# Performance work log

Measured on AMD Instinct MI355X. Metric: run time of the kernel, lower is better.

## Reference

```python
import jax, jax.numpy as jnp
import numpy as np

B, S, D, H, HD = 4, 2048, 1024, 16, 64


def setup_inputs() -> dict:
    key = jax.random.key(0)
    k1, k2, k3 = jax.random.split(key, 3)
    x = jax.random.normal(k1, (B, S, D), dtype=jnp.float32)
    w_attn = jax.random.normal(k2, (D, 3, H, HD), dtype=jnp.float32) * 0.02
    b_attn = jnp.zeros((3, H, HD), dtype=jnp.float32)
    w_proj = jax.random.normal(k3, (H, HD, D), dtype=jnp.float32) * 0.02
    b_proj = jnp.zeros((D,), dtype=jnp.float32)
    return {"x": x, "w_attn": w_attn, "b_attn": b_attn, "w_proj": w_proj, "b_proj": b_proj}


def reference(x, w_attn, b_attn, w_proj, b_proj):
    # c_attn: [B,S,D] x [D,3,H,HD] -> [B,3,H,S,HD]
    qkv = jnp.einsum('bsd,dqhe->bqhse', x, w_attn) + b_attn[None, :, :, None, :]
    q, k, v = qkv[:, 0], qkv[:, 1], qkv[:, 2]  # each [B,H,S,HD]
    scale = 1.0 / jnp.sqrt(jnp.asarray(HD, dtype=q.dtype))
    scores = jnp.einsum('bhse,bhte->bhst', q * scale, k)  # [B,H,S,S]
    causal = jnp.tril(jnp.ones((S, S), dtype=bool))
    scores = jnp.where(causal, scores, jnp.asarray(-1e9, dtype=scores.dtype))
    attn = jax.nn.softmax(scores, axis=-1)
    out = jnp.einsum('bhst,bhte->bhse', attn, v)  # [B,H,S,HD]
    # c_proj: contract (heads, head_size) -> embed
    return jnp.einsum('bhse,hed->bsd', out, w_proj) + b_proj
```

## Files before the change

### kernel.cpp

```cpp
#include <hip/hip_runtime.h>

#define NB 4
#define NS 2048
#define ND 1024
#define NH 16
#define NE 64
#define NM (NB*NS)

typedef __attribute__((ext_vector_type(8))) __bf16 bf16x8;
typedef __attribute__((ext_vector_type(4))) float f32x4;

__device__ __forceinline__ float bf2f(unsigned short h) {
  union { unsigned u; float f; } c; c.u = ((unsigned)h) << 16; return c.f;
}
__device__ __forceinline__ unsigned short f2bf(float f) {
  union { float f; unsigned u; } c; c.f = f;
  return (unsigned short)((c.u + 0x7fffu + ((c.u >> 16) & 1u)) >> 16);
}
__device__ __forceinline__ void load16_to_lds(const void* g, void* l) {
  __builtin_amdgcn_global_load_lds(
      (__attribute__((address_space(1))) void*)(void*)(unsigned long long)(const char*)g,
      (__attribute__((address_space(3))) void*)l, 16, 0, 0);
}

__global__ void detect_dtype(const unsigned* __restrict__ x, int* __restrict__ flag) {
  __shared__ int cnt;
  if (threadIdx.x == 0) cnt = 0;
  __syncthreads();
  unsigned w = x[((unsigned)threadIdx.x * 16381u) & ((1u << 21) - 1u)];
  unsigned lo = w & 0xFFFFu;
  int e = (int)((lo >> 7) & 0xFF);
  int plausible = (lo == 0u) || (e >= 100 && e <= 142);
  atomicAdd(&cnt, plausible);
  __syncthreads();
  if (threadIdx.x == 0) *flag = (cnt >= 192) ? 1 : 0;
}

__global__ void conv_to_bf16(const void* __restrict__ src, unsigned short* __restrict__ dst,
                             int n, const int* __restrict__ flag) {
  int stride = gridDim.x * blockDim.x;
  int i0 = blockIdx.x * blockDim.x + threadIdx.x;
  if (*flag) {
    const unsigned short* s = (const unsigned short*)src;
    for (int i = i0; i < n; i += stride) dst[i] = s[i];
  } else {
    const float* s = (const float*)src;
    for (int i = i0; i < n; i += stride) dst[i] = f2bf(s[i]);
  }
}

__global__ __launch_bounds__(256) void transpose_conv(const void* __restrict__ in,
                                                      unsigned short* __restrict__ out,
                                                      int K, int N, const int* __restrict__ flag) {
  __shared__ unsigned short tile[32][33];
  int n0 = blockIdx.x * 32, k0 = blockIdx.y * 32;
  int tx = threadIdx.x, ty = threadIdx.y;
  if (*flag) {
    const unsigned short* p = (const unsigned short*)in;
#pragma unroll
    for (int i = 0; i < 4; ++i)
      tile[ty + 8*i][tx] = p[(size_t)(k0 + ty + 8*i) * N + n0 + tx];
  } else {
    const float* p = (const float*)in;
#pragma unroll
    for (int i = 0; i < 4; ++i)
      tile[ty + 8*i][tx] = f2bf(p[(size_t)(k0 + ty + 8*i) * N + n0 + tx]);
  }
  __syncthreads();
#pragma unroll
  for (int i = 0; i < 4; ++i)
    out[(size_t)(n0 + ty + 8*i) * K + k0 + tx] = tile[tx][ty + 8*i];
}

#define SLOT_ELEMS ((256 + 128) * 64)

__device__ __forceinline__ void gemm_core_v3(const unsigned short* __restrict__ A,
                                             const unsigned short* __restrict__ Bt,
                                             int m0, int n0,
                                             unsigned short* sm,
                                             f32x4 (&acc)[4][4]) {
  const int t = threadIdx.x;
  const int lane = t & 63, w = t >> 6;
  const int wr = w >> 1, wc = w & 1;
  const int frm = lane & 15;
  const int p0 = ((lane >> 4) ^ (frm & 7)) * 8;

  auto stageA = [&](int kt, int slot) {
    unsigned short* Ab = sm + slot * SLOT_ELEMS;
    int kk = kt * 64;
#pragma unroll
    for (int u = 0; u < 4; ++u) {
      int ci = u * 512 + t;
      int r = ci >> 3, l = (ci & 7) ^ (r & 7);
      load16_to_lds(A + (size_t)(m0 + r) * ND + kk + l * 8, (char*)Ab + ci * 16);
    }
  };
  auto stageB = [&](int kt, int slot) {
    unsigned short* Bb = sm + slot * SLOT_ELEMS + 256 * 64;
    int kk = kt * 64;
#pragma unroll
    for (int u = 0; u < 2; ++u) {
      int ci = u * 512 + t;
      int r = ci >> 3, l = (ci & 7) ^ (r & 7);
      load16_to_lds(Bt + (size_t)(n0 + r) * ND + kk + l * 8, (char*)Bb + ci * 16);
    }
  };

  stageA(0, 0); stageB(0, 0);
  stageA(1, 1); stageB(1, 1);
  asm volatile("s_waitcnt vmcnt(6)\n\ts_barrier" ::: "memory");

  const int NT = ND / 64;
  for (int kt = 0; kt < NT; ++kt) {
    const unsigned short* Ab = sm + (kt % 3) * SLOT_ELEMS;
    const unsigned short* Bb = Ab + 256 * 64;
    const int ss = (kt + 2) % 3;
    const bool st = (kt + 2 < NT);

    bf16x8 a[4], b[4];
#pragma unroll
    for (int i = 0; i < 4; ++i)
      a[i] = *(const bf16x8*)(Ab + (64*wr + 16*i + frm) * 64 + p0);
#pragma unroll
    for (int j = 0; j < 4; ++j)
      b[j] = *(const bf16x8*)(Bb + (64*wc + 16*j + frm) * 64 + p0);
    if (st) stageA(kt + 2, ss);
    asm volatile("s_barrier" ::: "memory");
    asm volatile("s_waitcnt lgkmcnt(0)" ::: "memory");
    __builtin_amdgcn_s_setprio(1);
#pragma unroll
    for (int i = 0; i < 4; ++i)
#pragma unroll
      for (int j = 0; j < 4; ++j)
        acc[i][j] = __builtin_amdgcn_mfma_f32_16x16x32_bf16(a[i], b[j], acc[i][j], 0, 0, 0);
    __builtin_amdgcn_s_setprio(0);
    asm volatile("s_barrier" ::: "memory");

#pragma unroll
    for (int i = 0; i < 4; ++i)
      a[i] = *(const bf16x8*)(Ab + (64*wr + 16*i + frm) * 64 + (p0 ^ 32));
#pragma unroll
    for (int j = 0; j < 4; ++j)
      b[j] = *(const bf16x8*)(Bb + (64*wc + 16*j + frm) * 64 + (p0 ^ 32));
    if (st) stageB(kt + 2, ss);
    asm volatile("s_barrier" ::: "memory");
    asm volatile("s_waitcnt lgkmcnt(0)" ::: "memory");
    __builtin_amdgcn_s_setprio(1);
#pragma unroll
    for (int i = 0; i < 4; ++i)
#pragma unroll
      for (int j = 0; j < 4; ++j)
        acc[i][j] = __builtin_amdgcn_mfma_f32_16x16x32_bf16(a[i], b[j], acc[i][j], 0, 0, 0);
    __builtin_amdgcn_s_setprio(0);

    if (kt < NT - 2)       asm volatile("s_waitcnt vmcnt(6)\n\ts_barrier" ::: "memory");
    else if (kt == NT - 2) asm volatile("s_waitcnt vmcnt(0)\n\ts_barrier" ::: "memory");
  }
}

__global__ __launch_bounds__(512, 1) void gemm_qkv_v3(const unsigned short* __restrict__ X,
                                                      const unsigned short* __restrict__ W1T,
                                                      const unsigned short* __restrict__ battn,
                                                      unsigned short* __restrict__ qb,
                                                      unsigned short* __restrict__ kb,
                                                      unsigned short* __restrict__ vb) {
  __shared__ unsigned short sm[3 * SLOT_ELEMS];
  int flat = blockIdx.x + 24 * blockIdx.y;
  int virt = (flat & 7) * 96 + (flat >> 3);
  const int n0 = (virt % 24) * 128;
  const int m0 = (virt / 24) * 256;

  f32x4 acc[4][4] = {};
  gemm_core_v3(X, W1T, m0, n0, sm, acc);

  const int t = threadIdx.x, lane = t & 63, w = t >> 6;
  const int wr = w >> 1, wc = w & 1;
  const int coln = lane & 15, rbase = (lane >> 4) * 4;
#pragma unroll
  for (int j = 0; j < 4; ++j) {
    int nn = n0 + 64*wc + 16*j + coln;
    int qq = nn >> 10;
    int h  = (nn >> 6) & 15;
    int e  = nn & 63;
    float bias = bf2f(battn[nn]);
    unsigned short* dst = (qq == 0) ? qb : ((qq == 1) ? kb : vb);
    float scale = (qq == 0) ? (0.125f * 1.44269504f) : 1.0f;
#pragma unroll
    for (int i = 0; i < 4; ++i) {
#pragma unroll
      for (int rr = 0; rr < 4; ++rr) {
        int mm = m0 + 64*wr + 16*i + rbase + rr;
        int bb = mm >> 11, s = mm & 2047;
        float v = (acc[i][j][rr] + bias) * scale;
        size_t idx;
        if (qq == 2) idx = (((size_t)bb * NH + h) * NE + e) * NS + s;
        else         idx = (((size_t)bb * NH + h) * NS + s) * NE + e;
        dst[idx] = f2bf(v);
      }
    }
  }
}

__global__ __launch_bounds__(512, 1) void gemm_proj_v3(const unsigned short* __restrict__ A,
                                                       const unsigned short* __restrict__ W2T,
                                                       const unsigned short* __restrict__ bproj,
                                                       void* __restrict__ outv,
                                                       const int* __restrict__ flag) {
  __shared__ unsigned short sm[3 * SLOT_ELEMS];
  int flat = blockIdx.x + 8 * blockIdx.y;
  int virt = (flat & 7) * 32 + (flat >> 3);
  const int n0 = (virt % 8) * 128;
  const int m0 = (virt / 8) * 256;

  f32x4 acc[4][4] = {};
  gemm_core_v3(A, W2T, m0, n0, sm, acc);

  const int isbf = *flag;
  unsigned short* out16 = (unsigned short*)outv;
  float* out32 = (float*)outv;
  const int t = threadIdx.x, lane = t & 63, w = t >> 6;
  const int wr = w >> 1, wc = w & 1;
  const int coln = lane & 15, rbase = (lane >> 4) * 4;
#pragma unroll
  for (int j = 0; j < 4; ++j) {
    int nn = n0 + 64*wc + 16*j + coln;
    float bias = bf2f(bproj[nn]);
#pragma unroll
    for (int i = 0; i < 4; ++i) {
#pragma unroll
      for (int rr = 0; rr < 4; ++rr) {
        int mm = m0 + 64*wr + 16*i + rbase + rr;
        float v = acc[i][j][rr] + bias;
        if (isbf) out16[(size_t)mm * ND + nn] = f2bf(v);
        else      out32[(size_t)mm * ND + nn] = v;
      }
    }
  }
}

__global__ __launch_bounds__(256, 4) void attn_causal(const unsigned short* __restrict__ qb,
                                                      const unsigned short* __restrict__ kb,
                                                      const unsigned short* __restrict__ vtb,
                                                      unsigned short* __restrict__ ob) {
  __shared__ unsigned short QPs[128 * 64];
  __shared__ unsigned short Ks[2][32 * 64];
  __shared__ unsigned short Vt[2][32 * 64];

  int t = threadIdx.x, lane = t & 63, w = t >> 6;
  int qd = lane >> 4, li = lane & 15;
  int sw0 = ((qd ^ (li & 7)) * 8);
  int sw1 = (((4 + qd) ^ (li & 7)) * 8);

  const int qtab[4][4] = {{15,8,7,0},{14,9,6,1},{13,10,5,2},{12,11,4,3}};
  int bi = blockIdx.x;
  int bh = bi & 63;
  int qt = qtab[(bi >> 6) & 3][bi >> 8];
  int q0 = qt * 128;
  int NT = 4 * qt + 4;
  size_t base = (size_t)bh * NS * NE;
  int bb = bh >> 4, hh = bh & 15;

  bf16x8 onesf;
#pragma unroll
  for (int j = 0; j < 8; ++j) onesf[j] = (__bf16)1.0f;

  auto stage_kv = [&](int kt, int buf) {
    int k0 = kt * 32;
    int r = t >> 3, p = t & 7, l = p ^ (r & 7);
    load16_to_lds(kb + base + (size_t)(k0 + r) * NE + l * 8, (char*)Ks[buf] + t * 16);
    int e = 2 * r + (l >> 2);
    load16_to_lds(vtb + base + (size_t)e * NS + k0 + (l & 3) * 8, (char*)Vt[buf] + t * 16);
  };

#pragma unroll
  for (int c = 0; c < 4; ++c) {
    int ch = c * 256 + t;
    int r = ch >> 3, jl = (ch & 7) ^ (r & 7);
    load16_to_lds(qb + base + (size_t)(q0 + r) * NE + jl * 8, (char*)QPs + ch * 16);
  }
  stage_kv(0, 0);
  asm volatile("s_waitcnt vmcnt(2)\n\ts_barrier" ::: "memory");

  bf16x8 qa[2][2];
#pragma unroll
  for (int i = 0; i < 2; ++i) {
    const unsigned short* qr = QPs + (32*w + 16*i + li) * 64;
    qa[i][0] = *(const bf16x8*)(qr + sw0);
    qa[i][1] = *(const bf16x8*)(qr + sw1);
  }

  f32x4 o[2][4] = {};
  float l_run[2][4] = {};

  for (int kt = 0; kt < NT; ++kt) {
    int cur = kt & 1;
    asm volatile("s_waitcnt lgkmcnt(0)\n\ts_barrier" ::: "memory");
    if (kt + 1 < NT) {
      stage_kv(kt + 1, cur ^ 1);
      asm volatile("s_waitcnt vmcnt(2)\n\ts_barrier" ::: "memory");
    } else {
      asm volatile("s_waitcnt vmcnt(0)\n\ts_barrier" ::: "memory");
    }

    int k0 = kt * 32;
    const unsigned short* Ksc = Ks[cur];
    const unsigned short* Vtc = Vt[cur];

    bf16x8 kfr[2][2];
#pragma unroll
    for (int c = 0; c < 2; ++c) {
      const unsigned short* kr = Ksc + (16*c + li) * 64;
      kfr[c][0] = *(const bf16x8*)(kr + sw0);
      kfr[c][1] = *(const bf16x8*)(kr + sw1);
    }

    int need_mask = (k0 >= q0);
#pragma unroll
    for (int i = 0; i < 2; ++i) {
#pragma unroll
      for (int c = 0; c < 2; ++c) {
        f32x4 s = {};
        s = __builtin_amdgcn_mfma_f32_16x16x32_bf16(qa[i][0], kfr[c][0], s, 0, 0, 0);
        s = __builtin_amdgcn_mfma_f32_16x16x32_bf16(qa[i][1], kfr[c][1], s, 0, 0, 0);
#pragma unroll
        for (int rr = 0; rr < 4; ++rr) {
          float pv = exp2f(s[rr]);
          if (need_mask) {
            int colk = k0 + 16*c + li;
            int rowq = q0 + 32*w + 16*i + qd*4 + rr;
            if (colk > rowq) pv = 0.f;
          }
          int prow = 32*w + 16*i + qd*4 + rr;
          int lo = 2*c + (li >> 3);
          QPs[prow * 64 + ((lo ^ (prow & 7)) * 8) + (li & 7)] =
              (unsigned short)(__float_as_uint(pv) >> 16);
        }
      }
    }

    bf16x8 pa[2];
#pragma unroll
    for (int i = 0; i < 2; ++i)
      pa[i] = *(const bf16x8*)(QPs + (32*w + 16*i + li) * 64 + sw0);

#pragma unroll
    for (int i = 0; i < 2; ++i) {
      f32x4 sm = {};
      sm = __builtin_amdgcn_mfma_f32_16x16x32_bf16(pa[i], onesf, sm, 0, 0, 0);
#pragma unroll
      for (int rr = 0; rr < 4; ++rr) l_run[i][rr] += sm[rr];
    }

#pragma unroll
    for (int c2 = 0; c2 < 4; ++c2) {
      const unsigned short* vr = Vtc + (8*c2 + (li >> 1)) * 64;
      bf16x8 vf = *(const bf16x8*)(vr + ((((li & 1) * 4 + qd) ^ ((li >> 1) & 7)) * 8));
#pragma unroll
      for (int i = 0; i < 2; ++i)
        o[i][c2] = __builtin_amdgcn_mfma_f32_16x16x32_bf16(pa[i], vf, o[i][c2], 0, 0, 0);
    }
  }

#pragma unroll
  for (int i = 0; i < 2; ++i)
#pragma unroll
    for (int c = 0; c < 4; ++c)
#pragma unroll
      for (int rr = 0; rr < 4; ++rr) {
        int rowm = 32*w + 16*i + qd*4 + rr;
        float inv = 1.0f / fmaxf(l_run[i][rr], 1e-30f);
        float ov = o[i][c][rr] * inv;
        int e = 16*c + li;
        ob[(((size_t)bb * NS + (q0 + rowm)) * NH + hh) * NE + e] = f2bf(ov);
      }
}

extern "C" void kernel_launch(void* const* d_in, const int* in_sizes, int n_in,
                              void* d_out, int out_size, void* d_ws, size_t ws_size,
                              hipStream_t stream) {
  (void)in_sizes; (void)n_in; (void)out_size; (void)ws_size;
  char* ws = (char*)d_ws;
  unsigned short* W1T = (unsigned short*)(ws);
  unsigned short* W2T = (unsigned short*)(ws + 6291456);
  unsigned short* qb  = (unsigned short*)(ws + 8388608);
  unsigned short* kb  = (unsigned short*)(ws + 25165824);
  unsigned short* vb  = (unsigned short*)(ws + 41943040);
  unsigned short* ob  = (unsigned short*)(ws + 58720256);
  unsigned short* bac = (unsigned short*)(ws + 75497472);
  unsigned short* bpc = (unsigned short*)(ws + 75505664);
  int*            flg = (int*)(ws + 75513856);
  unsigned short* xc  = ob;

  detect_dtype<<<1, 256, 0, stream>>>((const unsigned*)d_in[0], flg);
  conv_to_bf16<<<2048, 256, 0, stream>>>(d_in[0], xc,  NB*NS*ND, flg);
  conv_to_bf16<<<12,   256, 0, stream>>>(d_in[2], bac, 3*NH*NE, flg);
  conv_to_bf16<<<4,    256, 0, stream>>>(d_in[4], bpc, ND, flg);

  transpose_conv<<<dim3(3072/32, 1024/32), dim3(32, 8), 0, stream>>>(d_in[1], W1T, 1024, 3072, flg);
  transpose_conv<<<dim3(1024/32, 1024/32), dim3(32, 8), 0, stream>>>(d_in[3], W2T, 1024, 1024, flg);
  gemm_qkv_v3<<<dim3(3072/128, NM/256), 512, 0, stream>>>(xc, W1T, bac, qb, kb, vb);
  attn_causal<<<dim3(1024), 256, 0, stream>>>(qb, kb, vb, ob);
  gemm_proj_v3<<<dim3(1024/128, NM/256), 512, 0, stream>>>(ob, W2T, bpc, d_out, flg);
}
```

Before: 288.1 us.

## Enlarge GEMM tiles to 256x256 with double-buffered half-tile staging

Replaces the 256x128 triple-buffered GEMM core with a 256x256 tile computed by 8 waves in a 2x4 layout, each owning a 128x64 sub-tile. LDS is double-buffered and refilled in halves interleaved across four MFMA sub-phases per k-step, raising arithmetic intensity per loaded byte. Grids for the QKV and projection GEMMs shrink by half, which cuts global traffic but leaves fewer blocks than CUs for the projection and a partial wave for QKV.

```diff
diff --git a/kernel.cpp b/kernel.cpp
--- a/kernel.cpp
+++ b/kernel.cpp
@@ -72,85 +72,140 @@
     out[(size_t)(n0 + ty + 8*i) * K + k0 + tx] = tile[tx][ty + 8*i];
 }
 
-#define SLOT_ELEMS ((256 + 128) * 64)
-
-__device__ __forceinline__ void gemm_core_v3(const unsigned short* __restrict__ A,
-                                             const unsigned short* __restrict__ Bt,
+
+__device__ __forceinline__ void gemm_core_v4(const unsigned short* __restrict__ Ag,
+                                             const unsigned short* __restrict__ Btg,
                                              int m0, int n0,
                                              unsigned short* sm,
-                                             f32x4 (&acc)[4][4]) {
+                                             f32x4 (&acc)[8][4]) {
+  char* smb = (char*)sm;
   const int t = threadIdx.x;
   const int lane = t & 63, w = t >> 6;
-  const int wr = w >> 1, wc = w & 1;
-  const int frm = lane & 15;
-  const int p0 = ((lane >> 4) ^ (frm & 7)) * 8;
-
-  auto stageA = [&](int kt, int slot) {
-    unsigned short* Ab = sm + slot * SLOT_ELEMS;
-    int kk = kt * 64;
-#pragma unroll
-    for (int u = 0; u < 4; ++u) {
-      int ci = u * 512 + t;
-      int r = ci >> 3, l = (ci & 7) ^ (r & 7);
-      load16_to_lds(A + (size_t)(m0 + r) * ND + kk + l * 8, (char*)Ab + ci * 16);
-    }
-  };
-  auto stageB = [&](int kt, int slot) {
-    unsigned short* Bb = sm + slot * SLOT_ELEMS + 256 * 64;
+  const int wr = w >> 2, wc = w & 3;
+  const int frm = lane & 15, qd = lane >> 4;
+  const int px0 = ((qd    ) ^ (frm & 7)) * 16;
+  const int px1 = ((4 + qd) ^ (frm & 7)) * 16;
+  const int NT = ND / 64;
+
+  auto stageAh = [&](int kt, int h) {
+    char* dst = smb + (kt & 1) * 65536;
     int kk = kt * 64;
 #pragma unroll
     for (int u = 0; u < 2; ++u) {
       int ci = u * 512 + t;
-      int r = ci >> 3, l = (ci & 7) ^ (r & 7);
-      load16_to_lds(Bt + (size_t)(n0 + r) * ND + kk + l * 8, (char*)Bb + ci * 16);
+      int rp = ci >> 3;
+      int row = ((rp >> 6) * 128) + h * 64 + (rp & 63);
+      int l = (ci & 7) ^ (row & 7);
+      load16_to_lds(Ag + (size_t)(m0 + row) * ND + kk + l * 8,
+                    dst + row * 128 + (ci & 7) * 16);
     }
   };
-
-  stageA(0, 0); stageB(0, 0);
-  stageA(1, 1); stageB(1, 1);
+  auto stageBh = [&](int kt, int h) {
+    char* dst = smb + (kt & 1) * 65536 + 32768;
+    int kk = kt * 64;
+#pragma unroll
+    for (int u = 0; u < 2; ++u) {
+      int ci = u * 512 + t;
+      int rp = ci >> 3;
+      int row = ((rp >> 5) * 64) + h * 32 + (rp & 31);
+      int l = (ci & 7) ^ (row & 7);
+      load16_to_lds(Btg + (size_t)(n0 + row) * ND + kk + l * 8,
+                    dst + row * 128 + (ci & 7) * 16);
+    }
+  };
+
+  stageAh(0, 0); stageAh(0, 1); stageBh(0, 0); stageBh(0, 1);
+  stageAh(1, 0); stageBh(1, 1); stageAh(1, 1);
   asm volatile("s_waitcnt vmcnt(6)\n\ts_barrier" ::: "memory");
 
-  const int NT = ND / 64;
   for (int kt = 0; kt < NT; ++kt) {
-    const unsigned short* Ab = sm + (kt % 3) * SLOT_ELEMS;
-    const unsigned short* Bb = Ab + 256 * 64;
-    const int ss = (kt + 2) % 3;
-    const bool st = (kt + 2 < NT);
-
-    bf16x8 a[4], b[4];
-#pragma unroll
-    for (int i = 0; i < 4; ++i)
-      a[i] = *(const bf16x8*)(Ab + (64*wr + 16*i + frm) * 64 + p0);
-#pragma unroll
-    for (int j = 0; j < 4; ++j)
-      b[j] = *(const bf16x8*)(Bb + (64*wc + 16*j + frm) * 64 + p0);
-    if (st) stageA(kt + 2, ss);
+    const char* Ab = smb + (kt & 1) * 65536;
+    const char* Bb = Ab + 32768;
+    bf16x8 a[4][2], b[2][2];
+
+#pragma unroll
+    for (int i = 0; i < 4; ++i) {
+      int row = 128*wr + 16*i + frm;
+      a[i][0] = *(const bf16x8*)(Ab + row * 128 + px0);
+      a[i][1] = *(const bf16x8*)(Ab + row * 128 + px1);
+    }
+#pragma unroll
+    for (int j = 0; j < 2; ++j) {
+      int row = 64*wc + 16*j + frm;
+      b[j][0] = *(const bf16x8*)(Bb + row * 128 + px0);
+      b[j][1] = *(const bf16x8*)(Bb + row * 128 + px1);
+    }
+    if (kt + 1 < NT) stageBh(kt + 1, 0);
     asm volatile("s_barrier" ::: "memory");
     asm volatile("s_waitcnt lgkmcnt(0)" ::: "memory");
     __builtin_amdgcn_s_setprio(1);
 #pragma unroll
     for (int i = 0; i < 4; ++i)
 #pragma unroll
-      for (int j = 0; j < 4; ++j)
-        acc[i][j] = __builtin_amdgcn_mfma_f32_16x16x32_bf16(a[i], b[j], acc[i][j], 0, 0, 0);
+      for (int j = 0; j < 2; ++j) {
+        acc[i][j] = __builtin_amdgcn_mfma_f32_16x16x32_bf16(a[i][0], b[j][0], acc[i][j], 0, 0, 0);
+        acc[i][j] = __builtin_amdgcn_mfma_f32_16x16x32_bf16(a[i][1], b[j][1], acc[i][j], 0, 0, 0);
+      }
     __builtin_amdgcn_s_setprio(0);
     asm volatile("s_barrier" ::: "memory");
 
 #pragma unroll
-    for (int i = 0; i < 4; ++i)
-      a[i] = *(const bf16x8*)(Ab + (64*wr + 16*i + frm) * 64 + (p0 ^ 32));
-#pragma unroll
-    for (int j = 0; j < 4; ++j)
-      b[j] = *(const bf16x8*)(Bb + (64*wc + 16*j + frm) * 64 + (p0 ^ 32));
-    if (st) stageB(kt + 2, ss);
+    for (int j = 0; j < 2; ++j) {
+      int row = 64*wc + 16*(2 + j) + frm;
+      b[j][0] = *(const bf16x8*)(Bb + row * 128 + px0);
+      b[j][1] = *(const bf16x8*)(Bb + row * 128 + px1);
+    }
+    if (kt + 2 < NT) stageAh(kt + 2, 0);
     asm volatile("s_barrier" ::: "memory");
     asm volatile("s_waitcnt lgkmcnt(0)" ::: "memory");
     __builtin_amdgcn_s_setprio(1);
 #pragma unroll
     for (int i = 0; i < 4; ++i)
 #pragma unroll
-      for (int j = 0; j < 4; ++j)
-        acc[i][j] = __builtin_amdgcn_mfma_f32_16x16x32_bf16(a[i], b[j], acc[i][j], 0, 0, 0);
+      for (int j = 0; j < 2; ++j) {
+        acc[i][2+j] = __builtin_amdgcn_mfma_f32_16x16x32_bf16(a[i][0], b[j][0], acc[i][2+j], 0, 0, 0);
+        acc[i][2+j] = __builtin_amdgcn_mfma_f32_16x16x32_bf16(a[i][1], b[j][1], acc[i][2+j], 0, 0, 0);
+      }
+    __builtin_amdgcn_s_setprio(0);
+    asm volatile("s_barrier" ::: "memory");
+
+#pragma unroll
+    for (int i = 0; i < 4; ++i) {
+      int row = 128*wr + 16*(4 + i) + frm;
+      a[i][0] = *(const bf16x8*)(Ab + row * 128 + px0);
+      a[i][1] = *(const bf16x8*)(Ab + row * 128 + px1);
+    }
+    if (kt + 2 < NT) stageBh(kt + 2, 1);
+    asm volatile("s_barrier" ::: "memory");
+    asm volatile("s_waitcnt lgkmcnt(0)" ::: "memory");
+    __builtin_amdgcn_s_setprio(1);
+#pragma unroll
+    for (int i = 0; i < 4; ++i)
+#pragma unroll
+      for (int j = 0; j < 2; ++j) {
+        acc[4+i][2+j] = __builtin_amdgcn_mfma_f32_16x16x32_bf16(a[i][0], b[j][0], acc[4+i][2+j], 0, 0, 0);
+        acc[4+i][2+j] = __builtin_amdgcn_mfma_f32_16x16x32_bf16(a[i][1], b[j][1], acc[4+i][2+j], 0, 0, 0);
+      }
+    __builtin_amdgcn_s_setprio(0);
+    asm volatile("s_barrier" ::: "memory");
+
+#pragma unroll
+    for (int j = 0; j < 2; ++j) {
+      int row = 64*wc + 16*j + frm;
+      b[j][0] = *(const bf16x8*)(Bb + row * 128 + px0);
+      b[j][1] = *(const bf16x8*)(Bb + row * 128 + px1);
+    }
+    if (kt + 2 < NT) stageAh(kt + 2, 1);
+    asm volatile("s_barrier" ::: "memory");
+    asm volatile("s_waitcnt lgkmcnt(0)" ::: "memory");
+    __builtin_amdgcn_s_setprio(1);
+#pragma unroll
+    for (int i = 0; i < 4; ++i)
+#pragma unroll
+      for (int j = 0; j < 2; ++j) {
+        acc[4+i][j] = __builtin_amdgcn_mfma_f32_16x16x32_bf16(a[i][0], b[j][0], acc[4+i][j], 0, 0, 0);
+        acc[4+i][j] = __builtin_amdgcn_mfma_f32_16x16x32_bf16(a[i][1], b[j][1], acc[4+i][j], 0, 0, 0);
+      }
     __builtin_amdgcn_s_setprio(0);
 
     if (kt < NT - 2)       asm volatile("s_waitcnt vmcnt(6)\n\ts_barrier" ::: "memory");
@@ -158,23 +213,23 @@
   }
 }
 
-__global__ __launch_bounds__(512, 1) void gemm_qkv_v3(const unsigned short* __restrict__ X,
+__global__ __launch_bounds__(512, 1) void gemm_qkv_v4(const unsigned short* __restrict__ X,
                                                       const unsigned short* __restrict__ W1T,
                                                       const unsigned short* __restrict__ battn,
                                                       unsigned short* __restrict__ qb,
                                                       unsigned short* __restrict__ kb,
                                                       unsigned short* __restrict__ vb) {
-  __shared__ unsigned short sm[3 * SLOT_ELEMS];
-  int flat = blockIdx.x + 24 * blockIdx.y;
-  int virt = (flat & 7) * 96 + (flat >> 3);
-  const int n0 = (virt % 24) * 128;
-  const int m0 = (virt / 24) * 256;
-
-  f32x4 acc[4][4] = {};
-  gemm_core_v3(X, W1T, m0, n0, sm, acc);
+  __shared__ unsigned short sm[2 * 2 * 256 * 64];
+  int flat = blockIdx.x + 12 * blockIdx.y;
+  int virt = (flat & 7) * 48 + (flat >> 3);
+  const int n0 = (virt % 12) * 256;
+  const int m0 = (virt / 12) * 256;
+
+  f32x4 acc[8][4] = {};
+  gemm_core_v4(X, W1T, m0, n0, sm, acc);
 
   const int t = threadIdx.x, lane = t & 63, w = t >> 6;
-  const int wr = w >> 1, wc = w & 1;
+  const int wr = w >> 2, wc = w & 3;
   const int coln = lane & 15, rbase = (lane >> 4) * 4;
 #pragma unroll
   for (int j = 0; j < 4; ++j) {
@@ -186,10 +241,10 @@
     unsigned short* dst = (qq == 0) ? qb : ((qq == 1) ? kb : vb);
     float scale = (qq == 0) ? (0.125f * 1.44269504f) : 1.0f;
 #pragma unroll
-    for (int i = 0; i < 4; ++i) {
+    for (int i = 0; i < 8; ++i) {
 #pragma unroll
       for (int rr = 0; rr < 4; ++rr) {
-        int mm = m0 + 64*wr + 16*i + rbase + rr;
+        int mm = m0 + 128*wr + 16*i + rbase + rr;
         int bb = mm >> 11, s = mm & 2047;
         float v = (acc[i][j][rr] + bias) * scale;
         size_t idx;
@@ -201,35 +256,35 @@
   }
 }
 
-__global__ __launch_bounds__(512, 1) void gemm_proj_v3(const unsigned short* __restrict__ A,
+__global__ __launch_bounds__(512, 1) void gemm_proj_v4(const unsigned short* __restrict__ A,
                                                        const unsigned short* __restrict__ W2T,
                                                        const unsigned short* __restrict__ bproj,
                                                        void* __restrict__ outv,
                                                        const int* __restrict__ flag) {
-  __shared__ unsigned short sm[3 * SLOT_ELEMS];
-  int flat = blockIdx.x + 8 * blockIdx.y;
-  int virt = (flat & 7) * 32 + (flat >> 3);
-  const int n0 = (virt % 8) * 128;
-  const int m0 = (virt / 8) * 256;
-
-  f32x4 acc[4][4] = {};
-  gemm_core_v3(A, W2T, m0, n0, sm, acc);
+  __shared__ unsigned short sm[2 * 2 * 256 * 64];
+  int flat = blockIdx.x + 4 * blockIdx.y;
+  int virt = (flat & 7) * 16 + (flat >> 3);
+  const int n0 = (virt & 3) * 256;
+  const int m0 = (virt >> 2) * 256;
+
+  f32x4 acc[8][4] = {};
+  gemm_core_v4(A, W2T, m0, n0, sm, acc);
 
   const int isbf = *flag;
   unsigned short* out16 = (unsigned short*)outv;
   float* out32 = (float*)outv;
   const int t = threadIdx.x, lane = t & 63, w = t >> 6;
-  const int wr = w >> 1, wc = w & 1;
+  const int wr = w >> 2, wc = w & 3;
   const int coln = lane & 15, rbase = (lane >> 4) * 4;
 #pragma unroll
   for (int j = 0; j < 4; ++j) {
     int nn = n0 + 64*wc + 16*j + coln;
     float bias = bf2f(bproj[nn]);
 #pragma unroll
-    for (int i = 0; i < 4; ++i) {
+    for (int i = 0; i < 8; ++i) {
 #pragma unroll
       for (int rr = 0; rr < 4; ++rr) {
-        int mm = m0 + 64*wr + 16*i + rbase + rr;
+        int mm = m0 + 128*wr + 16*i + rbase + rr;
         float v = acc[i][j][rr] + bias;
         if (isbf) out16[(size_t)mm * ND + nn] = f2bf(v);
         else      out32[(size_t)mm * ND + nn] = v;
@@ -398,7 +453,7 @@
 
   transpose_conv<<<dim3(3072/32, 1024/32), dim3(32, 8), 0, stream>>>(d_in[1], W1T, 1024, 3072, flg);
   transpose_conv<<<dim3(1024/32, 1024/32), dim3(32, 8), 0, stream>>>(d_in[3], W2T, 1024, 1024, flg);
-  gemm_qkv_v3<<<dim3(3072/128, NM/256), 512, 0, stream>>>(xc, W1T, bac, qb, kb, vb);
+  gemm_qkv_v4<<<dim3(3072/256, NM/256), 512, 0, stream>>>(xc, W1T, bac, qb, kb, vb);
   attn_causal<<<dim3(1024), 256, 0, stream>>>(qb, kb, vb, ob);
-  gemm_proj_v3<<<dim3(1024/128, NM/256), 512, 0, stream>>>(ob, W2T, bpc, d_out, flg);
-}
+  gemm_proj_v4<<<dim3(1024/256, NM/256), 512, 0, stream>>>(ob, W2T, bpc, d_out, flg);
+}
```

Result: slower. 309.1 us (+7.3%).

## Switch GEMM core to double-buffered LDS with two blocks per CU

Applied to the files above, without the earlier changes.

Replaces the three-slot, split-half GEMM pipeline with a two-buffer scheme. Each k-step issues the next tile's global-to-LDS loads up front, reads both k-halves of the fragments at once, runs all 32 MFMAs, then waits once on a barrier. LDS per block shrinks from 144KB to 96KB and launch bounds allow 2 blocks per CU, so occupancy can hide latency. The V-store epilogue also packs four bf16 values into one 64-bit store. The risk is that vmcnt(0) at every step exposes load latency, and raising occupancy limits registers per thread.

```diff
diff --git a/kernel.cpp b/kernel.cpp
--- a/kernel.cpp
+++ b/kernel.cpp
@@ -72,106 +72,92 @@
     out[(size_t)(n0 + ty + 8*i) * K + k0 + tx] = tile[tx][ty + 8*i];
 }
 
-#define SLOT_ELEMS ((256 + 128) * 64)
-
-__device__ __forceinline__ void gemm_core_v3(const unsigned short* __restrict__ A,
-                                             const unsigned short* __restrict__ Bt,
+#define BUFB 49152
+
+__device__ __forceinline__ void gemm_core_v5(const unsigned short* __restrict__ Ag,
+                                             const unsigned short* __restrict__ Btg,
                                              int m0, int n0,
                                              unsigned short* sm,
                                              f32x4 (&acc)[4][4]) {
+  char* smb = (char*)sm;
   const int t = threadIdx.x;
   const int lane = t & 63, w = t >> 6;
   const int wr = w >> 1, wc = w & 1;
-  const int frm = lane & 15;
-  const int p0 = ((lane >> 4) ^ (frm & 7)) * 8;
-
-  auto stageA = [&](int kt, int slot) {
-    unsigned short* Ab = sm + slot * SLOT_ELEMS;
+  const int frm = lane & 15, qd = lane >> 4;
+  const int px0 = ((qd    ) ^ (frm & 7)) * 16;
+  const int px1 = ((4 + qd) ^ (frm & 7)) * 16;
+  const int NT = ND / 64;
+
+  auto stage = [&](int kt, int b) {
+    char* Ab = smb + b * BUFB;
+    char* Bb = Ab + 32768;
     int kk = kt * 64;
 #pragma unroll
     for (int u = 0; u < 4; ++u) {
       int ci = u * 512 + t;
-      int r = ci >> 3, l = (ci & 7) ^ (r & 7);
-      load16_to_lds(A + (size_t)(m0 + r) * ND + kk + l * 8, (char*)Ab + ci * 16);
-    }
-  };
-  auto stageB = [&](int kt, int slot) {
-    unsigned short* Bb = sm + slot * SLOT_ELEMS + 256 * 64;
-    int kk = kt * 64;
+      int row = ci >> 3, c = ci & 7, l = c ^ (row & 7);
+      load16_to_lds(Ag + (size_t)(m0 + row) * ND + kk + l * 8, Ab + ci * 16);
+    }
 #pragma unroll
     for (int u = 0; u < 2; ++u) {
       int ci = u * 512 + t;
-      int r = ci >> 3, l = (ci & 7) ^ (r & 7);
-      load16_to_lds(Bt + (size_t)(n0 + r) * ND + kk + l * 8, (char*)Bb + ci * 16);
+      int row = ci >> 3, c = ci & 7, l = c ^ (row & 7);
+      load16_to_lds(Btg + (size_t)(n0 + row) * ND + kk + l * 8, Bb + ci * 16);
     }
   };
 
-  stageA(0, 0); stageB(0, 0);
-  stageA(1, 1); stageB(1, 1);
-  asm volatile("s_waitcnt vmcnt(6)\n\ts_barrier" ::: "memory");
-
-  const int NT = ND / 64;
+  stage(0, 0);
+  asm volatile("s_waitcnt vmcnt(0)\n\ts_barrier" ::: "memory");
+
   for (int kt = 0; kt < NT; ++kt) {
-    const unsigned short* Ab = sm + (kt % 3) * SLOT_ELEMS;
-    const unsigned short* Bb = Ab + 256 * 64;
-    const int ss = (kt + 2) % 3;
-    const bool st = (kt + 2 < NT);
-
-    bf16x8 a[4], b[4];
-#pragma unroll
-    for (int i = 0; i < 4; ++i)
-      a[i] = *(const bf16x8*)(Ab + (64*wr + 16*i + frm) * 64 + p0);
-#pragma unroll
-    for (int j = 0; j < 4; ++j)
-      b[j] = *(const bf16x8*)(Bb + (64*wc + 16*j + frm) * 64 + p0);
-    if (st) stageA(kt + 2, ss);
-    asm volatile("s_barrier" ::: "memory");
+    const int cur = kt & 1;
+    const char* Ab = smb + cur * BUFB;
+    const char* Bb = Ab + 32768;
+
+    if (kt + 1 < NT) stage(kt + 1, cur ^ 1);
+
+    bf16x8 a[4][2], b[4][2];
+#pragma unroll
+    for (int i = 0; i < 4; ++i) {
+      int row = 64*wr + 16*i + frm;
+      a[i][0] = *(const bf16x8*)(Ab + row * 128 + px0);
+      a[i][1] = *(const bf16x8*)(Ab + row * 128 + px1);
+    }
+#pragma unroll
+    for (int j = 0; j < 4; ++j) {
+      int row = 64*wc + 16*j + frm;
+      b[j][0] = *(const bf16x8*)(Bb + row * 128 + px0);
+      b[j][1] = *(const bf16x8*)(Bb + row * 128 + px1);
+    }
     asm volatile("s_waitcnt lgkmcnt(0)" ::: "memory");
     __builtin_amdgcn_s_setprio(1);
 #pragma unroll
     for (int i = 0; i < 4; ++i)
 #pragma unroll
-      for (int j = 0; j < 4; ++j)
-        acc[i][j] = __builtin_amdgcn_mfma_f32_16x16x32_bf16(a[i], b[j], acc[i][j], 0, 0, 0);
+      for (int j = 0; j < 4; ++j) {
+        acc[i][j] = __builtin_amdgcn_mfma_f32_16x16x32_bf16(a[i][0], b[j][0], acc[i][j], 0, 0, 0);
+        acc[i][j] = __builtin_amdgcn_mfma_f32_16x16x32_bf16(a[i][1], b[j][1], acc[i][j], 0, 0, 0);
+      }
     __builtin_amdgcn_s_setprio(0);
-    asm volatile("s_barrier" ::: "memory");
-
-#pragma unroll
-    for (int i = 0; i < 4; ++i)
-      a[i] = *(const bf16x8*)(Ab + (64*wr + 16*i + frm) * 64 + (p0 ^ 32));
-#pragma unroll
-    for (int j = 0; j < 4; ++j)
-      b[j] = *(const bf16x8*)(Bb + (64*wc + 16*j + frm) * 64 + (p0 ^ 32));
-    if (st) stageB(kt + 2, ss);
-    asm volatile("s_barrier" ::: "memory");
-    asm volatile("s_waitcnt lgkmcnt(0)" ::: "memory");
-    __builtin_amdgcn_s_setprio(1);
-#pragma unroll
-    for (int i = 0; i < 4; ++i)
-#pragma unroll
-      for (int j = 0; j < 4; ++j)
-        acc[i][j] = __builtin_amdgcn_mfma_f32_16x16x32_bf16(a[i], b[j], acc[i][j], 0, 0, 0);
-    __builtin_amdgcn_s_setprio(0);
-
-    if (kt < NT - 2)       asm volatile("s_waitcnt vmcnt(6)\n\ts_barrier" ::: "memory");
-    else if (kt == NT - 2) asm volatile("s_waitcnt vmcnt(0)\n\ts_barrier" ::: "memory");
-  }
-}
-
-__global__ __launch_bounds__(512, 1) void gemm_qkv_v3(const unsigned short* __restrict__ X,
+    if (kt + 1 < NT)
+      asm volatile("s_waitcnt vmcnt(0)\n\ts_barrier" ::: "memory");
+  }
+}
+
+__global__ __launch_bounds__(512, 2) void gemm_qkv_v5(const unsigned short* __restrict__ X,
                                                       const unsigned short* __restrict__ W1T,
                                                       const unsigned short* __restrict__ battn,
                                                       unsigned short* __restrict__ qb,
                                                       unsigned short* __restrict__ kb,
                                                       unsigned short* __restrict__ vb) {
-  __shared__ unsigned short sm[3 * SLOT_ELEMS];
+  __shared__ unsigned short sm[2 * 384 * 64];
   int flat = blockIdx.x + 24 * blockIdx.y;
   int virt = (flat & 7) * 96 + (flat >> 3);
   const int n0 = (virt % 24) * 128;
   const int m0 = (virt / 24) * 256;
 
   f32x4 acc[4][4] = {};
-  gemm_core_v3(X, W1T, m0, n0, sm, acc);
+  gemm_core_v5(X, W1T, m0, n0, sm, acc);
 
   const int t = threadIdx.x, lane = t & 63, w = t >> 6;
   const int wr = w >> 1, wc = w & 1;
@@ -183,37 +169,50 @@
     int h  = (nn >> 6) & 15;
     int e  = nn & 63;
     float bias = bf2f(battn[nn]);
-    unsigned short* dst = (qq == 0) ? qb : ((qq == 1) ? kb : vb);
     float scale = (qq == 0) ? (0.125f * 1.44269504f) : 1.0f;
-#pragma unroll
-    for (int i = 0; i < 4; ++i) {
-#pragma unroll
-      for (int rr = 0; rr < 4; ++rr) {
-        int mm = m0 + 64*wr + 16*i + rbase + rr;
-        int bb = mm >> 11, s = mm & 2047;
-        float v = (acc[i][j][rr] + bias) * scale;
-        size_t idx;
-        if (qq == 2) idx = (((size_t)bb * NH + h) * NE + e) * NS + s;
-        else         idx = (((size_t)bb * NH + h) * NS + s) * NE + e;
-        dst[idx] = f2bf(v);
-      }
-    }
-  }
-}
-
-__global__ __launch_bounds__(512, 1) void gemm_proj_v3(const unsigned short* __restrict__ A,
+    if (qq == 2) {
+#pragma unroll
+      for (int i = 0; i < 4; ++i) {
+        int mm0 = m0 + 64*wr + 16*i + rbase;
+        int bb = mm0 >> 11, s0 = mm0 & 2047;
+        unsigned long long pk = 0;
+#pragma unroll
+        for (int rr = 0; rr < 4; ++rr) {
+          float v = acc[i][j][rr] + bias;
+          pk |= ((unsigned long long)f2bf(v)) << (16 * rr);
+        }
+        size_t idx = (((size_t)bb * NH + h) * NE + e) * NS + s0;
+        *(unsigned long long*)(vb + idx) = pk;
+      }
+    } else {
+      unsigned short* dst = (qq == 0) ? qb : kb;
+#pragma unroll
+      for (int i = 0; i < 4; ++i) {
+#pragma unroll
+        for (int rr = 0; rr < 4; ++rr) {
+          int mm = m0 + 64*wr + 16*i + rbase + rr;
+          int bb = mm >> 11, s = mm & 2047;
+          float v = (acc[i][j][rr] + bias) * scale;
+          dst[(((size_t)bb * NH + h) * NS + s) * NE + e] = f2bf(v);
+        }
+      }
+    }
+  }
+}
+
+__global__ __launch_bounds__(512, 2) void gemm_proj_v5(const unsigned short* __restrict__ A,
                                                        const unsigned short* __restrict__ W2T,
                                                        const unsigned short* __restrict__ bproj,
                                                        void* __restrict__ outv,
                                                        const int* __restrict__ flag) {
-  __shared__ unsigned short sm[3 * SLOT_ELEMS];
+  __shared__ unsigned short sm[2 * 384 * 64];
   int flat = blockIdx.x + 8 * blockIdx.y;
   int virt = (flat & 7) * 32 + (flat >> 3);
   const int n0 = (virt % 8) * 128;
   const int m0 = (virt / 8) * 256;
 
   f32x4 acc[4][4] = {};
-  gemm_core_v3(A, W2T, m0, n0, sm, acc);
+  gemm_core_v5(A, W2T, m0, n0, sm, acc);
 
   const int isbf = *flag;
   unsigned short* out16 = (unsigned short*)outv;
@@ -398,7 +397,7 @@
 
   transpose_conv<<<dim3(3072/32, 1024/32), dim3(32, 8), 0, stream>>>(d_in[1], W1T, 1024, 3072, flg);
   transpose_conv<<<dim3(1024/32, 1024/32), dim3(32, 8), 0, stream>>>(d_in[3], W2T, 1024, 1024, flg);
-  gemm_qkv_v3<<<dim3(3072/128, NM/256), 512, 0, stream>>>(xc, W1T, bac, qb, kb, vb);
+  gemm_qkv_v5<<<dim3(3072/128, NM/256), 512, 0, stream>>>(xc, W1T, bac, qb, kb, vb);
   attn_causal<<<dim3(1024), 256, 0, stream>>>(qb, kb, vb, ob);
-  gemm_proj_v3<<<dim3(1024/128, NM/256), 512, 0, stream>>>(ob, W2T, bpc, d_out, flg);
-}
+  gemm_proj_v5<<<dim3(1024/128, NM/256), 512, 0, stream>>>(ob, W2T, bpc, d_out, flg);
+}
```

Result: faster. 263.4 us (-8.6%).
